# Kernel optimization log

Measured on AMD Instinct MI355X. Metric: run time of the kernel, lower is better.

## Reference

```python
import jax, jax.numpy as jnp
import numpy as np
import itertools


def _trilinear_interpn(vol, loc):
    """N-D linear interpolation of vol [*spatial, C] at locations loc [*spatial, N].
    Faithful to the torch module: floor/clamp corners, per-corner gather on the
    flattened volume, weights diff_loc1 = loc1 - loc, diff_loc0 = 1 - diff_loc1.
    """
    nb_dims = loc.shape[-1]
    spatial = vol.shape[:-1]
    C = vol.shape[-1]
    # row-major strides over spatial dims (k in the torch code)
    strides = np.cumprod((spatial[1:] + (1,))[::-1])[::-1]  # e.g. (H*W, W, 1) for 3D

    loc0 = jnp.floor(loc)
    max_loc = [d - 1 for d in spatial]
    loc0c = [jnp.clip(loc0[..., d], 0, max_loc[d]) for d in range(nb_dims)]
    loc1 = [jnp.clip(loc0c[d] + 1, 0, max_loc[d]) for d in range(nb_dims)]
    locs = [[f.astype(jnp.int32) for f in loc0c],
            [f.astype(jnp.int32) for f in loc1]]
    diff_loc1 = [loc1[d] - loc[..., d] for d in range(nb_dims)]
    diff_loc0 = [1.0 - d for d in diff_loc1]
    weights = [diff_loc1, diff_loc0]  # weights[0] pairs with loc0 corner, [1] with loc1

    vol_flat = vol.reshape(-1, C)
    interp = jnp.zeros(spatial + (C,), dtype=vol.dtype)
    for c in itertools.product([0, 1], repeat=nb_dims):
        subs = [locs[c[d]][d] for d in range(nb_dims)]
        idx = subs[0] * int(strides[0])
        for d in range(1, nb_dims):
            idx = idx + subs[d] * int(strides[d])
        vol_val = jnp.take(vol_flat, idx.reshape(-1), axis=0).reshape(spatial + (C,))
        wt = weights[c[0]][0]
        for d in range(1, nb_dims):
            wt = wt * weights[c[d]][d]
        interp = interp + wt[..., None] * vol_val
    return interp


def setup_inputs() -> dict:
    key = jax.random.key(0)
    k1, k2 = jax.random.split(key)
    D, H, W, C = 160, 192, 160, 4
    vol = jax.random.normal(k1, (D, H, W, C), dtype=jnp.float32)
    df = jax.random.normal(k2, (D, H, W, 3), dtype=jnp.float32)
    return {"vol": vol, "df": df}


def reference(vol, df):
    spatial = df.shape[:-1]
    nb_dims = len(spatial)
    # identity grid + displacement field -> absolute sample locations
    mesh = jnp.meshgrid(*[jnp.arange(d, dtype=jnp.float32) for d in spatial],
                        indexing="ij")
    loc = jnp.stack([mesh[d] + df[..., d] for d in range(nb_dims)], axis=-1)
    return _trilinear_interpn(vol, loc)
```

## Files before the change

kernel.cpp:

```cpp
#include <hip/hip_runtime.h>

#define D_ 160
#define H_ 192
#define W_ 160

__global__ __launch_bounds__(256) void st_trilinear_kernel(
    const float4* __restrict__ vol,
    const float*  __restrict__ df,
    float4*       __restrict__ out)
{
    int tid = threadIdx.x;
    int x = blockIdx.x * 16 + (tid & 15);
    int y = blockIdx.y * 4  + ((tid >> 4) & 3);
    int z = blockIdx.z * 4  + (tid >> 6);

    int idx = (z * H_ + y) * W_ + x;

    float dz = df[3 * idx + 0];
    float dy = df[3 * idx + 1];
    float dx = df[3 * idx + 2];

    float lz = (float)z + dz;
    float ly = (float)y + dy;
    float lx = (float)x + dx;

    float z0f = fminf(fmaxf(floorf(lz), 0.f), (float)(D_ - 1));
    float y0f = fminf(fmaxf(floorf(ly), 0.f), (float)(H_ - 1));
    float x0f = fminf(fmaxf(floorf(lx), 0.f), (float)(W_ - 1));
    float z1f = fminf(z0f + 1.f, (float)(D_ - 1));
    float y1f = fminf(y0f + 1.f, (float)(H_ - 1));
    float x1f = fminf(x0f + 1.f, (float)(W_ - 1));

    float wz0 = z1f - lz, wz1 = 1.f - wz0;
    float wy0 = y1f - ly, wy1 = 1.f - wy0;
    float wx0 = x1f - lx, wx1 = 1.f - wx0;

    int iz0 = (int)z0f, iz1 = (int)z1f;
    int iy0 = (int)y0f, iy1 = (int)y1f;
    int ix0 = (int)x0f, ix1 = (int)x1f;

    int b00 = (iz0 * H_ + iy0) * W_;
    int b01 = (iz0 * H_ + iy1) * W_;
    int b10 = (iz1 * H_ + iy0) * W_;
    int b11 = (iz1 * H_ + iy1) * W_;

    float4 v000 = vol[b00 + ix0];
    float4 v001 = vol[b00 + ix1];
    float4 v010 = vol[b01 + ix0];
    float4 v011 = vol[b01 + ix1];
    float4 v100 = vol[b10 + ix0];
    float4 v101 = vol[b10 + ix1];
    float4 v110 = vol[b11 + ix0];
    float4 v111 = vol[b11 + ix1];

    float w000 = wz0 * wy0 * wx0;
    float w001 = wz0 * wy0 * wx1;
    float w010 = wz0 * wy1 * wx0;
    float w011 = wz0 * wy1 * wx1;
    float w100 = wz1 * wy0 * wx0;
    float w101 = wz1 * wy0 * wx1;
    float w110 = wz1 * wy1 * wx0;
    float w111 = wz1 * wy1 * wx1;

    float4 r;
    r.x = w000 * v000.x + w001 * v001.x + w010 * v010.x + w011 * v011.x
        + w100 * v100.x + w101 * v101.x + w110 * v110.x + w111 * v111.x;
    r.y = w000 * v000.y + w001 * v001.y + w010 * v010.y + w011 * v011.y
        + w100 * v100.y + w101 * v101.y + w110 * v110.y + w111 * v111.y;
    r.z = w000 * v000.z + w001 * v001.z + w010 * v010.z + w011 * v011.z
        + w100 * v100.z + w101 * v101.z + w110 * v110.z + w111 * v111.z;
    r.w = w000 * v000.w + w001 * v001.w + w010 * v010.w + w011 * v011.w
        + w100 * v100.w + w101 * v101.w + w110 * v110.w + w111 * v111.w;

    out[idx] = r;
}

extern "C" void kernel_launch(void* const* d_in, const int* in_sizes, int n_in,
                              void* d_out, int out_size, void* d_ws, size_t ws_size,
                              hipStream_t stream) {
    const float4* vol = (const float4*)d_in[0];
    const float*  df  = (const float*)d_in[1];
    float4* out = (float4*)d_out;

    dim3 grid(W_ / 16, H_ / 4, D_ / 4);
    st_trilinear_kernel<<<grid, 256, 0, stream>>>(vol, df, out);
}
```

Before: 231.0 us.

## Stage halo tile of volume in shared memory for trilinear gathers

Each 8x8x8 output block first loads a 16x16x15 halo region of the volume (clamped at the borders) into shared memory, then performs the eight corner reads from LDS when the sample falls inside the tile, falling back to global gathers otherwise. The goal is to replace scattered global/L2 gathers with LDS reads, since displacements are standard-normal and mostly small. The cost is loading roughly 7x more voxels than outputs per block, plus a sync and lower occupancy from about 61KB of LDS per block.

```diff
diff --git a/kernel.cpp b/kernel.cpp
--- a/kernel.cpp
+++ b/kernel.cpp
@@ -4,16 +4,34 @@
 #define H_ 192
 #define W_ 160
 
-__global__ __launch_bounds__(256) void st_trilinear_kernel(
+#define EX 16
+#define EY 16
+#define EZ 15
+#define TILE_N (EX * EY * EZ)
+
+__global__ __launch_bounds__(512, 4) void st_trilinear_kernel(
     const float4* __restrict__ vol,
     const float*  __restrict__ df,
     float4*       __restrict__ out)
 {
+    __shared__ float4 tile[TILE_N];
+
     int tid = threadIdx.x;
-    int x = blockIdx.x * 16 + (tid & 15);
-    int y = blockIdx.y * 4  + ((tid >> 4) & 3);
-    int z = blockIdx.z * 4  + (tid >> 6);
+    int bx0 = blockIdx.x * 8, by0 = blockIdx.y * 8, bz0 = blockIdx.z * 8;
+    int rx0 = bx0 - 4, ry0 = by0 - 4, rz0 = bz0 - 4;
 
+    for (int s = tid; s < TILE_N; s += 512) {
+        int sx = s & 15, sy = (s >> 4) & 15, sz = s >> 8;
+        int gx = min(max(rx0 + sx, 0), W_ - 1);
+        int gy = min(max(ry0 + sy, 0), H_ - 1);
+        int gz = min(max(rz0 + sz, 0), D_ - 1);
+        tile[s] = vol[(gz * H_ + gy) * W_ + gx];
+    }
+    __syncthreads();
+
+    int x = bx0 + (tid & 7);
+    int y = by0 + ((tid >> 3) & 7);
+    int z = bz0 + (tid >> 6);
     int idx = (z * H_ + y) * W_ + x;
 
     float dz = df[3 * idx + 0];
@@ -39,19 +57,38 @@
     int iy0 = (int)y0f, iy1 = (int)y1f;
     int ix0 = (int)x0f, ix1 = (int)x1f;
 
-    int b00 = (iz0 * H_ + iy0) * W_;
-    int b01 = (iz0 * H_ + iy1) * W_;
-    int b10 = (iz1 * H_ + iy0) * W_;
-    int b11 = (iz1 * H_ + iy1) * W_;
+    float4 v000, v001, v010, v011, v100, v101, v110, v111;
 
-    float4 v000 = vol[b00 + ix0];
-    float4 v001 = vol[b00 + ix1];
-    float4 v010 = vol[b01 + ix0];
-    float4 v011 = vol[b01 + ix1];
-    float4 v100 = vol[b10 + ix0];
-    float4 v101 = vol[b10 + ix1];
-    float4 v110 = vol[b11 + ix0];
-    float4 v111 = vol[b11 + ix1];
+    bool inTile = (ix0 >= rx0) && (ix1 <= rx0 + EX - 1) &&
+                  (iy0 >= ry0) && (iy1 <= ry0 + EY - 1) &&
+                  (iz0 >= rz0) && (iz1 <= rz0 + EZ - 1);
+
+    if (inTile) {
+        int lx0 = ix0 - rx0,        lx1 = ix1 - rx0;
+        int ly0 = (iy0 - ry0) << 4, ly1 = (iy1 - ry0) << 4;
+        int lz0 = (iz0 - rz0) << 8, lz1 = (iz1 - rz0) << 8;
+        v000 = tile[lz0 + ly0 + lx0];
+        v001 = tile[lz0 + ly0 + lx1];
+        v010 = tile[lz0 + ly1 + lx0];
+        v011 = tile[lz0 + ly1 + lx1];
+        v100 = tile[lz1 + ly0 + lx0];
+        v101 = tile[lz1 + ly0 + lx1];
+        v110 = tile[lz1 + ly1 + lx0];
+        v111 = tile[lz1 + ly1 + lx1];
+    } else {
+        int b00 = (iz0 * H_ + iy0) * W_;
+        int b01 = (iz0 * H_ + iy1) * W_;
+        int b10 = (iz1 * H_ + iy0) * W_;
+        int b11 = (iz1 * H_ + iy1) * W_;
+        v000 = vol[b00 + ix0];
+        v001 = vol[b00 + ix1];
+        v010 = vol[b01 + ix0];
+        v011 = vol[b01 + ix1];
+        v100 = vol[b10 + ix0];
+        v101 = vol[b10 + ix1];
+        v110 = vol[b11 + ix0];
+        v111 = vol[b11 + ix1];
+    }
 
     float w000 = wz0 * wy0 * wx0;
     float w001 = wz0 * wy0 * wx1;
@@ -82,6 +119,6 @@
     const float*  df  = (const float*)d_in[1];
     float4* out = (float4*)d_out;
 
-    dim3 grid(W_ / 16, H_ / 4, D_ / 4);
-    st_trilinear_kernel<<<grid, 256, 0, stream>>>(vol, df, out);
+    dim3 grid(W_ / 8, H_ / 8, D_ / 8);
+    st_trilinear_kernel<<<grid, 512, 0, stream>>>(vol, df, out);
 }
```

After: 252.2 us. 9.2% more time.
